# Kernel optimization log

Hardware: AMD Instinct MI355X
Metric: run time of the kernel (lower is better)

Reference implementation:

```python
import jax, jax.numpy as jnp
from jax import lax
import numpy as np

B, H, W = 8, 512, 512
HW = H * W  # sentinel label for non-mask pixels


def _label_components(mask):
    """4-connectivity connected-component labeling (min flat-index per component).
    mask: [H,W] bool. Returns [HW] int32 labels; non-mask pixels get label HW.
    Label propagation + pointer jumping -> O(log diameter) iterations."""
    idx = jnp.arange(HW, dtype=jnp.int32).reshape(H, W)
    lab0 = jnp.where(mask, idx, HW)

    def step(lab):
        p = jnp.pad(lab, 1, mode='constant', constant_values=HW)
        nb = jnp.minimum(jnp.minimum(p[:-2, 1:-1], p[2:, 1:-1]),
                         jnp.minimum(p[1:-1, :-2], p[1:-1, 2:]))
        new = jnp.where(mask, jnp.minimum(lab, nb), HW)
        flat = new.reshape(-1)
        flat_ext = jnp.concatenate([flat, jnp.array([HW], dtype=flat.dtype)])
        new = jnp.minimum(flat, flat_ext[flat]).reshape(H, W)  # pointer jump
        return jnp.where(mask, new, HW)

    def cond(state):
        return state[1]

    def body(state):
        lab, _ = state
        new = step(lab)
        return new, jnp.any(new != lab)

    lab, _ = lax.while_loop(cond, body, (lab0, jnp.array(True)))
    return lab.reshape(-1)


def _keep_large(mask):
    """Keep pixels belonging to components with area > max_area/2 (matches
    ndi.label + ndi.sum + thresholded relabel; ndi.sum scaling by 255/1 cancels)."""
    labels = _label_components(mask)  # [HW]
    counts = jax.ops.segment_sum(mask.reshape(-1).astype(jnp.float32), labels,
                                 num_segments=HW + 1)  # counts[HW]=0 (non-mask contributes 0)
    max_area = counts.max()
    keep = mask.reshape(-1) & (counts[labels] > 0.5 * max_area)
    return keep.reshape(mask.shape)


def _masked_ce(logits, target):
    """CrossEntropyLoss(ignore_index=255, reduction='mean'). logits [B,C,H,W], target [B,H,W]."""
    logp = jax.nn.log_softmax(logits, axis=1)
    valid = target != 255
    tc = jnp.where(valid, target, 0)
    nll = -jnp.take_along_axis(logp, tc[:, None], axis=1)[:, 0]  # [B,H,W]
    denom = jnp.maximum(jnp.sum(valid), 1).astype(logp.dtype)
    return jnp.sum(jnp.where(valid, nll, 0.0)) / denom


def setup_inputs() -> dict:
    key = jax.random.key(0)
    k1, k2 = jax.random.split(key)
    preds = jax.random.normal(k1, (3, B, 2, H, W), dtype=jnp.float32)
    cams = jax.random.uniform(k2, (B, 1, H, W), dtype=jnp.float32)
    return {"preds": preds, "cams": cams}


def reference(preds, cams):
    cam = cams[:, 0]                      # [B,H,W]
    bg_mask = cam >= 0.2                  # pixels left at 255 in bg_label (the labeled regions)
    fg_mask = cam > 0.6                   # pixels set to 1 in fg_label
    keep_bg = jax.vmap(_keep_large)(bg_mask)
    keep_fg = jax.vmap(_keep_large)(fg_mask)
    bg_t = jnp.where(keep_bg, 255, 0).astype(jnp.int32)   # large uncertain regions ignored
    fg_t = jnp.where(keep_fg, 1, 255).astype(jnp.int32)   # small/non-fg ignored
    loss = jnp.float32(0.0)
    for i in range(preds.shape[0]):       # weight (1**i / 1) == 1
        loss = loss + _masked_ce(preds[i], fg_t) + _masked_ce(preds[i], bg_t)
    return loss
```

## Files before the change

### kernel.cpp

```cpp
#include <hip/hip_runtime.h>
#include <hip/hip_bf16.h>
#include <math.h>

#define Bsz    8
#define Wdim   512
#define HWv    (512 * 512)
#define LOG2HW 18
#define NIMG   16
#define TILE   64
#define TPIX   (TILE * TILE)
#define NTILE  (NIMG * 64)
#define LCAP   2048
#define CEBLK  6144
#define CNTBLK 2048
#define NBORD  448


__device__ __forceinline__ int uf_find(int* L, int x) {
  int p = L[x];
  while (p != x) {
    int gp = L[p];
    if (gp != p) atomicMin(&L[x], gp);
    x = gp;
    p = L[x];
  }
  return x;
}

__device__ __forceinline__ int find_ro(const int* __restrict__ L, int x) {
  int p = L[x];
  while (p != x) { x = p; p = L[x]; }
  return x;
}

__device__ __forceinline__ void uf_union(int* L, int a, int b) {
  a = uf_find(L, a);
  b = uf_find(L, b);
  while (a != b) {
    if (a < b) { int t = a; a = b; b = t; }
    int old = atomicMin(&L[a], b);
    if (old == a) return;
    a = old;
  }
}


__global__ __launch_bounds__(512) void k_local(const float* __restrict__ cams,
                                               int* __restrict__ labels,
                                               int* __restrict__ rootlist,
                                               int* __restrict__ rootcnt) {
  int img  = blockIdx.x >> 6;
  int tile = blockIdx.x & 63;
  int tY = tile >> 3, tX = tile & 7;
  int b = img & 7;
  bool fg = (img & 8) != 0;
  int gbase = img << LOG2HW;
  int oy = tY * TILE, ox = tX * TILE;
  int lane = threadIdx.x & 63;

  __shared__ int P[TPIX];
  __shared__ int A[TPIX];
  __shared__ int lcount;
  if (threadIdx.x == 0) lcount = 0;

  #pragma unroll
  for (int it = 0; it < 8; ++it) {
    int i  = it * 512 + threadIdx.x;
    int ly = i >> 6;
    float c = cams[(b << LOG2HW) + ((oy + ly) << 9) + (ox + lane)];
    bool m = fg ? (c > 0.6f) : (c >= 0.2f);
    unsigned long long bm = __ballot(m);
    int par = -1;
    if (m) {
      unsigned long long below = (1ULL << lane) - 1ULL;
      unsigned long long z = (~bm) & below;
      int rs = z ? (64 - __clzll(z)) : 0;
      par = (ly << 6) + rs;
    }
    P[i] = par;
    A[i] = 0;
  }
  __syncthreads();

  #pragma unroll
  for (int it = 0; it < 8; ++it) {
    int i = it * 512 + threadIdx.x;
    if (i >= TILE && P[i] >= 0 && P[i - TILE] >= 0) {
      bool skip = (lane > 0) && (P[i - 1] >= 0) && (P[i - TILE - 1] >= 0);
      if (!skip) uf_union(P, i, i - TILE);
    }
  }
  __syncthreads();

  #pragma unroll
  for (int it = 0; it < 8; ++it) {
    int i = it * 512 + threadIdx.x;
    bool m = P[i] >= 0;
    unsigned long long bm = __ballot(m);
    int rs = 0;
    if (m) {
      unsigned long long below = (1ULL << lane) - 1ULL;
      unsigned long long z = (~bm) & below;
      rs = z ? (64 - __clzll(z)) : 0;
    }
    bool isStart = m && (rs == lane);
    int r = -1;
    if (isStart) r = find_ro(P, i);
    int root = __shfl(r, rs);
    if (m) P[i] = root;
    if (isStart) {
      unsigned long long t = (~bm) >> lane;
      int runlen = t ? (__ffsll((long long)t) - 1) : (64 - lane);
      atomicAdd(&A[root], runlen);
    }
  }
  __syncthreads();

  int lbase = blockIdx.x << 11;
  #pragma unroll
  for (int it = 0; it < 8; ++it) {
    int i  = it * 512 + threadIdx.x;
    int ly = i >> 6;
    int g  = ((oy + ly) << 9) + (ox + lane);
    int p  = P[i];
    int lab = -1;
    if (p >= 0) lab = ((oy + (p >> 6)) << 9) + (ox + (p & 63));
    labels[gbase + g] = lab;
    if (p == i) {
      int pos = atomicAdd(&lcount, 1);
      rootlist[lbase + pos] = (A[i] << 12) | i;
    }
  }
  __syncthreads();
  if (threadIdx.x == 0) rootcnt[blockIdx.x] = lcount;
}

__global__ void k_border(int* __restrict__ labels, int* __restrict__ maxa,
                         const int* __restrict__ rootlist,
                         const int* __restrict__ rootcnt,
                         int* __restrict__ areasF) {
  if (blockIdx.x >= NBORD) {
    int tileg = blockIdx.x - NBORD;
    int img  = tileg >> 6;
    int tile = tileg & 63;
    int tY = tile >> 3, tX = tile & 7;
    int oy = tY * TILE, ox = tX * TILE;
    int cnt = rootcnt[tileg];
    int lbase = tileg << 11;
    for (int e = threadIdx.x; e < cnt; e += 256) {
      int i = rootlist[lbase + e] & 4095;
      int g = ((oy + (i >> 6)) << 9) + (ox + (i & 63));
      areasF[(img << LOG2HW) + g] = 0;
    }
    return;
  }
  if (blockIdx.x == 0) {
    if (threadIdx.x < NIMG) maxa[threadIdx.x] = 0;
  }
  const int per_img = 14 * Wdim;
  int t = blockIdx.x * blockDim.x + threadIdx.x;
  if (t >= NIMG * per_img) return;
  int img = t / per_img;
  int r   = t - img * per_img;
  int k = r >> 9, j = r & (Wdim - 1);
  int* L = labels + (img << LOG2HW);
  if (k < 7) {
    int x = TILE * k + (TILE - 1);
    int p = (j << 9) + x, q = p + 1;
    if (L[p] >= 0 && L[q] >= 0) {
      bool skip = (j > 0) && (L[p - Wdim] >= 0) && (L[q - Wdim] >= 0);
      if (!skip) uf_union(L, p, q);
    }
  } else {
    int y = TILE * (k - 7) + (TILE - 1);
    int p = (y << 9) + j, q = p + Wdim;
    if (L[p] >= 0 && L[q] >= 0) {
      bool skip = (j > 0) && (L[p - 1] >= 0) && (L[q - 1] >= 0);
      if (!skip) uf_union(L, p, q);
    }
  }
}

__global__ __launch_bounds__(256) void k_flat2(int* __restrict__ labels,
                                               const int* __restrict__ rootlist,
                                               const int* __restrict__ rootcnt,
                                               int* __restrict__ areasF,
                                               int* __restrict__ maxa) {
  int tileg = blockIdx.x;
  int img  = tileg >> 6;
  int tile = tileg & 63;
  int tY = tile >> 3, tX = tile & 7;
  int oy = tY * TILE, ox = tX * TILE;
  int cnt = rootcnt[tileg];
  int lbase = tileg << 11;
  int* L = labels + (img << LOG2HW);
  int* AF = areasF + (img << LOG2HW);
  int mymax = 0;
  for (int e = threadIdx.x; e < cnt; e += 256) {
    int ent  = rootlist[lbase + e];
    int i    = ent & 4095;
    int area = ent >> 12;
    int g = ((oy + (i >> 6)) << 9) + (ox + (i & 63));
    int fr = find_ro(L, g);
    L[g] = fr;
    int prev = atomicAdd(&AF[fr], area);
    mymax = max(mymax, prev + area);
  }
  #pragma unroll
  for (int off = 32; off > 0; off >>= 1)
    mymax = max(mymax, __shfl_down(mymax, off));
  __shared__ int lm[4];
  int wave = threadIdx.x >> 6;
  if ((threadIdx.x & 63) == 0) lm[wave] = mymax;
  __syncthreads();
  if (threadIdx.x == 0) {
    int bm = max(max(lm[0], lm[1]), max(lm[2], lm[3]));
    if (bm > 0) atomicMax(&maxa[img], bm);
  }
}

__global__ __launch_bounds__(256) void k_verd_root(const int* __restrict__ labels,
                                                   const int* __restrict__ rootlist,
                                                   const int* __restrict__ rootcnt,
                                                   const int* __restrict__ areasF,
                                                   const int* __restrict__ maxa,
                                                   unsigned char* __restrict__ verdictB) {
  int tileg = blockIdx.x;
  int img  = tileg >> 6;
  int tile = tileg & 63;
  int tY = tile >> 3, tX = tile & 7;
  int oy = tY * TILE, ox = tX * TILE;
  int cnt = rootcnt[tileg];
  int lbase = tileg << 11;
  int mx = maxa[img];
  const int* L  = labels + (img << LOG2HW);
  const int* AF = areasF + (img << LOG2HW);
  for (int e = threadIdx.x; e < cnt; e += 256) {
    int i = rootlist[lbase + e] & 4095;
    int g = ((oy + (i >> 6)) << 9) + (ox + (i & 63));
    int tot = AF[L[g]];
    verdictB[(img << LOG2HW) + g] = (2 * tot > mx) ? 1 : 0;
  }
}

__global__ __launch_bounds__(256) void k_vbits(const int* __restrict__ labels,
                                               const unsigned char* __restrict__ verdictB,
                                               unsigned long long* __restrict__ bitsBG,
                                               unsigned long long* __restrict__ bitsFG) {
  int tid = blockIdx.x * 256 + threadIdx.x;
  int img = tid >> 16;
  int g4  = tid & 65535;
  int4 lb = *(const int4*)&labels[(img << LOG2HW) + (g4 << 2)];
  const unsigned char* V = verdictB + (img << LOG2HW);
  unsigned nib = 0;
  if (lb.x >= 0) nib |= (unsigned)V[lb.x];
  if (lb.y >= 0) nib |= (unsigned)V[lb.y] << 1;
  if (lb.z >= 0) nib |= (unsigned)V[lb.z] << 2;
  if (lb.w >= 0) nib |= (unsigned)V[lb.w] << 3;

  int lane = threadIdx.x & 63;
  unsigned long long w = (unsigned long long)nib << ((lane & 15) << 2);
  w |= __shfl_xor(w, 1);
  w |= __shfl_xor(w, 2);
  w |= __shfl_xor(w, 4);
  w |= __shfl_xor(w, 8);
  if ((lane & 15) == 0) {
    int wordIdx = g4 >> 4;
    unsigned long long* dst = (img < 8) ? (bitsBG + ((img & 7) << 12))
                                        : (bitsFG + ((img & 7) << 12));
    dst[wordIdx] = w;
  }
}

__global__ __launch_bounds__(256) void k_ce(const float* __restrict__ preds,
                                            const unsigned long long* __restrict__ bitsBG,
                                            const unsigned long long* __restrict__ bitsFG,
                                            float* __restrict__ pf,
                                            float* __restrict__ pbg,
                                            int* __restrict__ pcf,
                                            int* __restrict__ pcb) {
  int tid = blockIdx.x * 256 + threadIdx.x;
  int g4  = tid & 65535;
  int pb  = tid >> 16;
  int b   = pb & 7;
  int p   = pb >> 3;

  int wi = (b << 12) + (g4 >> 4);
  int sh = (g4 & 15) << 2;
  unsigned nB = (unsigned)(bitsBG[wi] >> sh) & 15u;
  unsigned nF = (unsigned)(bitsFG[wi] >> sh) & 15u;

  const float* pbase = preds + ((size_t)((p * Bsz + b) * 2) << LOG2HW);
  int px = g4 << 2;
  float4 A0 = *(const float4*)&pbase[px];
  float4 A1 = *(const float4*)&pbase[HWv + px];

  float d[4] = {A0.x - A1.x, A0.y - A1.y, A0.z - A1.z, A0.w - A1.w};
  float sfg = 0.f, sbg = 0.f;
  #pragma unroll
  for (int j = 0; j < 4; ++j) {
    float sp = logf(1.f + expf(-fabsf(d[j])));
    bool vfj = (nF >> j) & 1u;
    bool vbj = !((nB >> j) & 1u);
    sfg += vfj ? (fmaxf(d[j], 0.f) + sp) : 0.f;
    sbg += vbj ? (fmaxf(-d[j], 0.f) + sp) : 0.f;
  }
  int cf = __popc(nF);
  int cb = 4 - __popc(nB);

  #pragma unroll
  for (int off = 32; off > 0; off >>= 1) {
    sfg += __shfl_down(sfg, off);
    sbg += __shfl_down(sbg, off);
    cf  += __shfl_down(cf, off);
    cb  += __shfl_down(cb, off);
  }
  __shared__ float lsf[4], lsb[4];
  __shared__ int   lcf[4], lcb[4];
  int wave = threadIdx.x >> 6;
  if ((threadIdx.x & 63) == 0) {
    lsf[wave] = sfg; lsb[wave] = sbg; lcf[wave] = cf; lcb[wave] = cb;
  }
  __syncthreads();
  if (threadIdx.x == 0) {
    pf[blockIdx.x]  = lsf[0] + lsf[1] + lsf[2] + lsf[3];
    pbg[blockIdx.x] = lsb[0] + lsb[1] + lsb[2] + lsb[3];
    if (p == 0) {
      pcf[blockIdx.x] = lcf[0] + lcf[1] + lcf[2] + lcf[3];
      pcb[blockIdx.x] = lcb[0] + lcb[1] + lcb[2] + lcb[3];
    }
  }
}

__global__ __launch_bounds__(1024) void k_final(const float* __restrict__ pf,
                                                const float* __restrict__ pbg,
                                                const int* __restrict__ pcf,
                                                const int* __restrict__ pcb,
                                                float* __restrict__ out) {
  int t = threadIdx.x;
  double sf = 0.0, sb = 0.0;
  int cf = 0, cb = 0;
  #pragma unroll
  for (int k = 0; k < CEBLK / 1024; ++k) {
    sf += (double)pf[k * 1024 + t];
    sb += (double)pbg[k * 1024 + t];
  }
  #pragma unroll
  for (int k = 0; k < CNTBLK / 1024; ++k) {
    cf += pcf[k * 1024 + t];
    cb += pcb[k * 1024 + t];
  }
  #pragma unroll
  for (int off = 32; off > 0; off >>= 1) {
    sf += __shfl_down(sf, off);
    sb += __shfl_down(sb, off);
    cf += __shfl_down(cf, off);
    cb += __shfl_down(cb, off);
  }
  __shared__ double dsf[16], dsb[16];
  __shared__ int    icf[16], icb[16];
  int wave = t >> 6;
  if ((t & 63) == 0) { dsf[wave] = sf; dsb[wave] = sb; icf[wave] = cf; icb[wave] = cb; }
  __syncthreads();
  if (t == 0) {
    double tf = 0.0, tb = 0.0; int af_ = 0, ab_ = 0;
    #pragma unroll
    for (int w = 0; w < 16; ++w) { tf += dsf[w]; tb += dsb[w]; af_ += icf[w]; ab_ += icb[w]; }
    double df = af_ > 0 ? (double)af_ : 1.0;
    double db = ab_ > 0 ? (double)ab_ : 1.0;
    out[0] = (float)(tf / df + tb / db);
  }
}

extern "C" void kernel_launch(void* const* d_in, const int* in_sizes, int n_in,
                              void* d_out, int out_size, void* d_ws, size_t ws_size,
                              hipStream_t stream) {
  (void)in_sizes; (void)n_in; (void)out_size; (void)ws_size;
  const float* preds = (const float*)d_in[0];
  const float* cams  = (const float*)d_in[1];
  float* out = (float*)d_out;

  int* labels = (int*)d_ws;
  int* areasF = labels + NIMG * HWv;
  int* maxa   = areasF + NIMG * HWv;
  double* sums = (double*)(maxa + 16);
  int* counts  = (int*)(sums + 2);
  unsigned long long* bitsBG = (unsigned long long*)(counts + 2);
  unsigned long long* bitsFG = bitsBG + Bsz * (HWv / 64);
  float* pf  = (float*)(bitsFG + Bsz * (HWv / 64));
  float* pbg = pf + CEBLK;
  int*   pcf = (int*)(pbg + CEBLK);
  int*   pcb = pcf + CNTBLK;
  int*   rootlist = pcb + CNTBLK;
  int*   rootcnt  = rootlist + NTILE * LCAP;
  unsigned char* verdictB = (unsigned char*)(rootcnt + NTILE);

  const int threads = 256;

  k_local    <<<NTILE, 512, 0, stream>>>(cams, labels, rootlist, rootcnt);
  k_border   <<<NBORD + NTILE, threads, 0, stream>>>(labels, maxa, rootlist, rootcnt, areasF);
  k_flat2    <<<NTILE, threads, 0, stream>>>(labels, rootlist, rootcnt, areasF, maxa);
  k_verd_root<<<NTILE, threads, 0, stream>>>(labels, rootlist, rootcnt, areasF, maxa, verdictB);
  k_vbits    <<<NIMG * HWv / 4 / threads, threads, 0, stream>>>(labels, verdictB, bitsBG, bitsFG);
  k_ce       <<<CEBLK, threads, 0, stream>>>(preds, bitsBG, bitsFG, pf, pbg, pcf, pcb);
  k_final    <<<1, 1024, 0, stream>>>(pf, pbg, pcf, pcb, out);
}
```

Measured before the change: 157.1 us.

## Use 64x32 tiles, fuse verdict and bit-packing, and widen CE per-thread work

Tiles shrink from 64x64 to 64x32 with 256-thread blocks, doubling the tile count and adding more horizontal border rows for the union kernel. The areasF zeroing and maxa init move into k_local, with wave-aggregated rootlist appends, so k_border now only does border unions. Verdict computation and bitmask packing are merged into one per-tile kernel that stages verdicts in shared memory, removing the global byte verdict array and one launch. k_ce now handles 8 pixels per thread with half the blocks, and k_final sums counts with one load per thread. The intent is fewer launches and less global traffic, at the cost of more border merging and a different occupancy mix.

```diff
diff --git a/kernel.cpp b/kernel.cpp
--- a/kernel.cpp
+++ b/kernel.cpp
@@ -7,13 +7,14 @@
 #define HWv    (512 * 512)
 #define LOG2HW 18
 #define NIMG   16
-#define TILE   64
-#define TPIX   (TILE * TILE)
-#define NTILE  (NIMG * 64)
-#define LCAP   2048
-#define CEBLK  6144
-#define CNTBLK 2048
-#define NBORD  448
+#define TW     64
+#define TH     32
+#define TPIX   (TW * TH)
+#define NTILE  (NIMG * 128)
+#define LCAP   1024
+#define CEBLK  3072
+#define CNTBLK 1024
+#define NBORD  704
 
 
 __device__ __forceinline__ int uf_find(int* L, int x) {
@@ -45,27 +46,30 @@
 }
 
 
-__global__ __launch_bounds__(512) void k_local(const float* __restrict__ cams,
-                                               int* __restrict__ labels,
-                                               int* __restrict__ rootlist,
-                                               int* __restrict__ rootcnt) {
-  int img  = blockIdx.x >> 6;
-  int tile = blockIdx.x & 63;
-  int tY = tile >> 3, tX = tile & 7;
+__global__ __launch_bounds__(256, 8) void k_local(const float* __restrict__ cams,
+                                                  int* __restrict__ labels,
+                                                  int* __restrict__ areasF,
+                                                  int* __restrict__ maxa,
+                                                  int* __restrict__ rootlist,
+                                                  int* __restrict__ rootcnt) {
+  int img  = blockIdx.x >> 7;
+  int tile = blockIdx.x & 127;
+  int tS = tile >> 3, tX = tile & 7;
   int b = img & 7;
   bool fg = (img & 8) != 0;
   int gbase = img << LOG2HW;
-  int oy = tY * TILE, ox = tX * TILE;
+  int oy = tS * TH, ox = tX * TW;
   int lane = threadIdx.x & 63;
 
   __shared__ int P[TPIX];
   __shared__ int A[TPIX];
   __shared__ int lcount;
   if (threadIdx.x == 0) lcount = 0;
+  if (blockIdx.x == 0 && threadIdx.x < NIMG) maxa[threadIdx.x] = 0;
 
   #pragma unroll
   for (int it = 0; it < 8; ++it) {
-    int i  = it * 512 + threadIdx.x;
+    int i  = it * 256 + threadIdx.x;
     int ly = i >> 6;
     float c = cams[(b << LOG2HW) + ((oy + ly) << 9) + (ox + lane)];
     bool m = fg ? (c > 0.6f) : (c >= 0.2f);
@@ -84,17 +88,17 @@
 
   #pragma unroll
   for (int it = 0; it < 8; ++it) {
-    int i = it * 512 + threadIdx.x;
-    if (i >= TILE && P[i] >= 0 && P[i - TILE] >= 0) {
-      bool skip = (lane > 0) && (P[i - 1] >= 0) && (P[i - TILE - 1] >= 0);
-      if (!skip) uf_union(P, i, i - TILE);
+    int i = it * 256 + threadIdx.x;
+    if (i >= TW && P[i] >= 0 && P[i - TW] >= 0) {
+      bool skip = (lane > 0) && (P[i - 1] >= 0) && (P[i - TW - 1] >= 0);
+      if (!skip) uf_union(P, i, i - TW);
     }
   }
   __syncthreads();
 
   #pragma unroll
   for (int it = 0; it < 8; ++it) {
-    int i = it * 512 + threadIdx.x;
+    int i = it * 256 + threadIdx.x;
     bool m = P[i] >= 0;
     unsigned long long bm = __ballot(m);
     int rs = 0;
@@ -116,48 +120,34 @@
   }
   __syncthreads();
 
-  int lbase = blockIdx.x << 11;
+  int lbase = blockIdx.x << 10;
   #pragma unroll
   for (int it = 0; it < 8; ++it) {
-    int i  = it * 512 + threadIdx.x;
+    int i  = it * 256 + threadIdx.x;
     int ly = i >> 6;
     int g  = ((oy + ly) << 9) + (ox + lane);
     int p  = P[i];
     int lab = -1;
     if (p >= 0) lab = ((oy + (p >> 6)) << 9) + (ox + (p & 63));
     labels[gbase + g] = lab;
-    if (p == i) {
-      int pos = atomicAdd(&lcount, 1);
-      rootlist[lbase + pos] = (A[i] << 12) | i;
+    bool isRoot = (p == i);
+    unsigned long long bm = __ballot(isRoot);
+    int nr = __popcll(bm);
+    int basepos = 0;
+    if (lane == 0 && nr) basepos = atomicAdd(&lcount, nr);
+    basepos = __shfl(basepos, 0);
+    if (isRoot) {
+      int off = (int)__popcll(bm & ((1ULL << lane) - 1ULL));
+      rootlist[lbase + basepos + off] = (A[i] << 12) | i;
+      areasF[gbase + g] = 0;
     }
   }
   __syncthreads();
   if (threadIdx.x == 0) rootcnt[blockIdx.x] = lcount;
 }
 
-__global__ void k_border(int* __restrict__ labels, int* __restrict__ maxa,
-                         const int* __restrict__ rootlist,
-                         const int* __restrict__ rootcnt,
-                         int* __restrict__ areasF) {
-  if (blockIdx.x >= NBORD) {
-    int tileg = blockIdx.x - NBORD;
-    int img  = tileg >> 6;
-    int tile = tileg & 63;
-    int tY = tile >> 3, tX = tile & 7;
-    int oy = tY * TILE, ox = tX * TILE;
-    int cnt = rootcnt[tileg];
-    int lbase = tileg << 11;
-    for (int e = threadIdx.x; e < cnt; e += 256) {
-      int i = rootlist[lbase + e] & 4095;
-      int g = ((oy + (i >> 6)) << 9) + (ox + (i & 63));
-      areasF[(img << LOG2HW) + g] = 0;
-    }
-    return;
-  }
-  if (blockIdx.x == 0) {
-    if (threadIdx.x < NIMG) maxa[threadIdx.x] = 0;
-  }
-  const int per_img = 14 * Wdim;
+__global__ void k_border(int* __restrict__ labels) {
+  const int per_img = 22 * Wdim;
   int t = blockIdx.x * blockDim.x + threadIdx.x;
   if (t >= NIMG * per_img) return;
   int img = t / per_img;
@@ -165,14 +155,14 @@
   int k = r >> 9, j = r & (Wdim - 1);
   int* L = labels + (img << LOG2HW);
   if (k < 7) {
-    int x = TILE * k + (TILE - 1);
+    int x = TW * k + (TW - 1);
     int p = (j << 9) + x, q = p + 1;
     if (L[p] >= 0 && L[q] >= 0) {
       bool skip = (j > 0) && (L[p - Wdim] >= 0) && (L[q - Wdim] >= 0);
       if (!skip) uf_union(L, p, q);
     }
   } else {
-    int y = TILE * (k - 7) + (TILE - 1);
+    int y = TH * (k - 7) + (TH - 1);
     int p = (y << 9) + j, q = p + Wdim;
     if (L[p] >= 0 && L[q] >= 0) {
       bool skip = (j > 0) && (L[p - 1] >= 0) && (L[q - 1] >= 0);
@@ -187,12 +177,12 @@
                                                int* __restrict__ areasF,
                                                int* __restrict__ maxa) {
   int tileg = blockIdx.x;
-  int img  = tileg >> 6;
-  int tile = tileg & 63;
-  int tY = tile >> 3, tX = tile & 7;
-  int oy = tY * TILE, ox = tX * TILE;
+  int img  = tileg >> 7;
+  int tile = tileg & 127;
+  int tS = tile >> 3, tX = tile & 7;
+  int oy = tS * TH, ox = tX * TW;
   int cnt = rootcnt[tileg];
-  int lbase = tileg << 11;
+  int lbase = tileg << 10;
   int* L = labels + (img << LOG2HW);
   int* AF = areasF + (img << LOG2HW);
   int mymax = 0;
@@ -219,86 +209,83 @@
   }
 }
 
-__global__ __launch_bounds__(256) void k_verd_root(const int* __restrict__ labels,
-                                                   const int* __restrict__ rootlist,
-                                                   const int* __restrict__ rootcnt,
-                                                   const int* __restrict__ areasF,
-                                                   const int* __restrict__ maxa,
-                                                   unsigned char* __restrict__ verdictB) {
+__global__ __launch_bounds__(256) void k_vmerge(const int* __restrict__ labels,
+                                                const int* __restrict__ rootlist,
+                                                const int* __restrict__ rootcnt,
+                                                const int* __restrict__ areasF,
+                                                const int* __restrict__ maxa,
+                                                unsigned long long* __restrict__ bitsBG,
+                                                unsigned long long* __restrict__ bitsFG) {
   int tileg = blockIdx.x;
-  int img  = tileg >> 6;
-  int tile = tileg & 63;
-  int tY = tile >> 3, tX = tile & 7;
-  int oy = tY * TILE, ox = tX * TILE;
+  int img  = tileg >> 7;
+  int tile = tileg & 127;
+  int tS = tile >> 3, tX = tile & 7;
+  int oy = tS * TH, ox = tX * TW;
   int cnt = rootcnt[tileg];
-  int lbase = tileg << 11;
+  int lbase = tileg << 10;
   int mx = maxa[img];
   const int* L  = labels + (img << LOG2HW);
   const int* AF = areasF + (img << LOG2HW);
+
+  __shared__ unsigned char V[TPIX];
   for (int e = threadIdx.x; e < cnt; e += 256) {
     int i = rootlist[lbase + e] & 4095;
     int g = ((oy + (i >> 6)) << 9) + (ox + (i & 63));
-    int tot = AF[L[g]];
-    verdictB[(img << LOG2HW) + g] = (2 * tot > mx) ? 1 : 0;
-  }
-}
-
-__global__ __launch_bounds__(256) void k_vbits(const int* __restrict__ labels,
-                                               const unsigned char* __restrict__ verdictB,
-                                               unsigned long long* __restrict__ bitsBG,
-                                               unsigned long long* __restrict__ bitsFG) {
+    V[i] = (2 * AF[L[g]] > mx) ? 1 : 0;
+  }
+  __syncthreads();
+
+  unsigned long long* dst = (img < 8) ? (bitsBG + ((img & 7) << 12))
+                                      : (bitsFG + ((img & 7) << 12));
+  #pragma unroll
+  for (int it = 0; it < 2; ++it) {
+    int grp = it * 256 + threadIdx.x;
+    int row = grp >> 4;
+    int4 lb = *(const int4*)&L[((oy + row) << 9) + ox + ((grp & 15) << 2)];
+    unsigned nib = 0;
+    if (lb.x >= 0) nib |= (unsigned)V[(((lb.x >> 9) & 31) << 6) | (lb.x & 63)];
+    if (lb.y >= 0) nib |= (unsigned)V[(((lb.y >> 9) & 31) << 6) | (lb.y & 63)] << 1;
+    if (lb.z >= 0) nib |= (unsigned)V[(((lb.z >> 9) & 31) << 6) | (lb.z & 63)] << 2;
+    if (lb.w >= 0) nib |= (unsigned)V[(((lb.w >> 9) & 31) << 6) | (lb.w & 63)] << 3;
+    unsigned long long w = (unsigned long long)nib << ((grp & 15) << 2);
+    w |= __shfl_xor(w, 1);
+    w |= __shfl_xor(w, 2);
+    w |= __shfl_xor(w, 4);
+    w |= __shfl_xor(w, 8);
+    if ((threadIdx.x & 15) == 0) dst[((oy + row) << 3) + tX] = w;
+  }
+}
+
+__global__ __launch_bounds__(256, 8) void k_ce(const float* __restrict__ preds,
+                                               const unsigned long long* __restrict__ bitsBG,
+                                               const unsigned long long* __restrict__ bitsFG,
+                                               float* __restrict__ pf,
+                                               float* __restrict__ pbg,
+                                               int* __restrict__ pcf,
+                                               int* __restrict__ pcb) {
   int tid = blockIdx.x * 256 + threadIdx.x;
-  int img = tid >> 16;
-  int g4  = tid & 65535;
-  int4 lb = *(const int4*)&labels[(img << LOG2HW) + (g4 << 2)];
-  const unsigned char* V = verdictB + (img << LOG2HW);
-  unsigned nib = 0;
-  if (lb.x >= 0) nib |= (unsigned)V[lb.x];
-  if (lb.y >= 0) nib |= (unsigned)V[lb.y] << 1;
-  if (lb.z >= 0) nib |= (unsigned)V[lb.z] << 2;
-  if (lb.w >= 0) nib |= (unsigned)V[lb.w] << 3;
-
-  int lane = threadIdx.x & 63;
-  unsigned long long w = (unsigned long long)nib << ((lane & 15) << 2);
-  w |= __shfl_xor(w, 1);
-  w |= __shfl_xor(w, 2);
-  w |= __shfl_xor(w, 4);
-  w |= __shfl_xor(w, 8);
-  if ((lane & 15) == 0) {
-    int wordIdx = g4 >> 4;
-    unsigned long long* dst = (img < 8) ? (bitsBG + ((img & 7) << 12))
-                                        : (bitsFG + ((img & 7) << 12));
-    dst[wordIdx] = w;
-  }
-}
-
-__global__ __launch_bounds__(256) void k_ce(const float* __restrict__ preds,
-                                            const unsigned long long* __restrict__ bitsBG,
-                                            const unsigned long long* __restrict__ bitsFG,
-                                            float* __restrict__ pf,
-                                            float* __restrict__ pbg,
-                                            int* __restrict__ pcf,
-                                            int* __restrict__ pcb) {
-  int tid = blockIdx.x * 256 + threadIdx.x;
-  int g4  = tid & 65535;
-  int pb  = tid >> 16;
+  int g8  = tid & 32767;
+  int pb  = tid >> 15;
   int b   = pb & 7;
   int p   = pb >> 3;
 
-  int wi = (b << 12) + (g4 >> 4);
-  int sh = (g4 & 15) << 2;
-  unsigned nB = (unsigned)(bitsBG[wi] >> sh) & 15u;
-  unsigned nF = (unsigned)(bitsFG[wi] >> sh) & 15u;
+  int wi = (b << 12) + (g8 >> 3);
+  int sh = (g8 & 7) << 3;
+  unsigned nB = (unsigned)(bitsBG[wi] >> sh) & 255u;
+  unsigned nF = (unsigned)(bitsFG[wi] >> sh) & 255u;
 
   const float* pbase = preds + ((size_t)((p * Bsz + b) * 2) << LOG2HW);
-  int px = g4 << 2;
-  float4 A0 = *(const float4*)&pbase[px];
-  float4 A1 = *(const float4*)&pbase[HWv + px];
-
-  float d[4] = {A0.x - A1.x, A0.y - A1.y, A0.z - A1.z, A0.w - A1.w};
+  int px = g8 << 3;
+  float4 A0a = *(const float4*)&pbase[px];
+  float4 A0b = *(const float4*)&pbase[px + 4];
+  float4 A1a = *(const float4*)&pbase[HWv + px];
+  float4 A1b = *(const float4*)&pbase[HWv + px + 4];
+
+  float d[8] = {A0a.x - A1a.x, A0a.y - A1a.y, A0a.z - A1a.z, A0a.w - A1a.w,
+                A0b.x - A1b.x, A0b.y - A1b.y, A0b.z - A1b.z, A0b.w - A1b.w};
   float sfg = 0.f, sbg = 0.f;
   #pragma unroll
-  for (int j = 0; j < 4; ++j) {
+  for (int j = 0; j < 8; ++j) {
     float sp = logf(1.f + expf(-fabsf(d[j])));
     bool vfj = (nF >> j) & 1u;
     bool vbj = !((nB >> j) & 1u);
@@ -306,7 +293,7 @@
     sbg += vbj ? (fmaxf(-d[j], 0.f) + sp) : 0.f;
   }
   int cf = __popc(nF);
-  int cb = 4 - __popc(nB);
+  int cb = 8 - __popc(nB);
 
   #pragma unroll
   for (int off = 32; off > 0; off >>= 1) {
@@ -339,17 +326,13 @@
                                                 float* __restrict__ out) {
   int t = threadIdx.x;
   double sf = 0.0, sb = 0.0;
-  int cf = 0, cb = 0;
   #pragma unroll
   for (int k = 0; k < CEBLK / 1024; ++k) {
     sf += (double)pf[k * 1024 + t];
     sb += (double)pbg[k * 1024 + t];
   }
-  #pragma unroll
-  for (int k = 0; k < CNTBLK / 1024; ++k) {
-    cf += pcf[k * 1024 + t];
-    cb += pcb[k * 1024 + t];
-  }
+  int cf = pcf[t];
+  int cb = pcb[t];
   #pragma unroll
   for (int off = 32; off > 0; off >>= 1) {
     sf += __shfl_down(sf, off);
@@ -393,15 +376,13 @@
   int*   pcb = pcf + CNTBLK;
   int*   rootlist = pcb + CNTBLK;
   int*   rootcnt  = rootlist + NTILE * LCAP;
-  unsigned char* verdictB = (unsigned char*)(rootcnt + NTILE);
 
   const int threads = 256;
 
-  k_local    <<<NTILE, 512, 0, stream>>>(cams, labels, rootlist, rootcnt);
-  k_border   <<<NBORD + NTILE, threads, 0, stream>>>(labels, maxa, rootlist, rootcnt, areasF);
-  k_flat2    <<<NTILE, threads, 0, stream>>>(labels, rootlist, rootcnt, areasF, maxa);
-  k_verd_root<<<NTILE, threads, 0, stream>>>(labels, rootlist, rootcnt, areasF, maxa, verdictB);
-  k_vbits    <<<NIMG * HWv / 4 / threads, threads, 0, stream>>>(labels, verdictB, bitsBG, bitsFG);
-  k_ce       <<<CEBLK, threads, 0, stream>>>(preds, bitsBG, bitsFG, pf, pbg, pcf, pcb);
-  k_final    <<<1, 1024, 0, stream>>>(pf, pbg, pcf, pcb, out);
-}
+  k_local  <<<NTILE, threads, 0, stream>>>(cams, labels, areasF, maxa, rootlist, rootcnt);
+  k_border <<<NBORD, threads, 0, stream>>>(labels);
+  k_flat2  <<<NTILE, threads, 0, stream>>>(labels, rootlist, rootcnt, areasF, maxa);
+  k_vmerge <<<NTILE, threads, 0, stream>>>(labels, rootlist, rootcnt, areasF, maxa, bitsBG, bitsFG);
+  k_ce     <<<CEBLK, threads, 0, stream>>>(preds, bitsBG, bitsFG, pf, pbg, pcf, pcb);
+  k_final  <<<1, 1024, 0, stream>>>(pf, pbg, pcf, pcb, out);
+}
```

Result: slower. 165.1 us (+5.1%).
